# Performance work log

Hardware: AMD Instinct MI355X
Metric: run time of the kernel (lower is better)

The kernel has to match this reference:

```python
import jax, jax.numpy as jnp
import numpy as np

FP8_E4M3_MAX = 448.0  # torch.float8_e4m3fn max


def _fp8_quant(x, scale):
    # per-tensor static-scale fp8 quantization: clamp(x/scale) -> e4m3 -> back to f32
    q = jnp.clip(x / scale, -FP8_E4M3_MAX, FP8_E4M3_MAX)
    return q.astype(jnp.float8_e4m3fn).astype(jnp.float32)


def setup_inputs() -> dict:
    key = jax.random.key(0)
    k1, k2, k3 = jax.random.split(key, 3)
    M, K, N = 8192, 4096, 11008
    inp = jax.random.normal(k1, (M, K), dtype=jnp.float32)
    # weight is stored pre-quantized (fp8 values held as fp32), already transposed to [K, N]
    w = jax.random.normal(k2, (K, N), dtype=jnp.float32) * 0.02
    weight_scale = jnp.float32(0.01)
    qweight = _fp8_quant(w, weight_scale)
    qbias = jax.random.normal(k3, (N,), dtype=jnp.float32) * 0.01
    input_scale = jnp.float32(0.05)
    return {
        "input": inp,
        "qweight": qweight,
        "qbias": qbias,
        "weight_scale": weight_scale,
        "input_scale": input_scale,
    }


def reference(input, qweight, qbias, weight_scale, input_scale) -> jnp.ndarray:
    # scaled_fp8_quant with a provided static scale: x_scale == input_scale
    qinput = _fp8_quant(input, input_scale)  # [M, K], fp8 values in f32
    # cutlass_scaled_mm / _scaled_mm: (qinput * x_scale) @ (qweight * weight_scale) + bias
    out = jnp.einsum("mk,kn->mn", qinput, qweight) * (input_scale * weight_scale)
    out = out + qbias[None, :]
    return out.astype(input.dtype)
```

## Files before the change

kernel.cpp:

```cpp
#include <hip/hip_runtime.h>

typedef float v4f __attribute__((ext_vector_type(4)));
typedef unsigned long long u64x2 __attribute__((ext_vector_type(2)));

#define BM 128
#define BN 128
#define BK 64

__device__ __forceinline__ unsigned int pack4_fp8(float a, float b, float c, float d) {
    unsigned int v = __builtin_amdgcn_cvt_pk_fp8_f32(a, b, 0, false);
    v = __builtin_amdgcn_cvt_pk_fp8_f32(c, d, v, true);
    return v;
}

__global__ __launch_bounds__(256) void quant_x_kernel(
    const float* __restrict__ X, const float* __restrict__ sp,
    unsigned int* __restrict__ Q)
{
    const long i = (long)blockIdx.x * 256 + threadIdx.x;
    const float s = sp[0];
    const float4 v = ((const float4*)X)[i];
    const float a = fminf(fmaxf(v.x / s, -448.f), 448.f);
    const float b = fminf(fmaxf(v.y / s, -448.f), 448.f);
    const float c = fminf(fmaxf(v.z / s, -448.f), 448.f);
    const float d = fminf(fmaxf(v.w / s, -448.f), 448.f);
    Q[i] = pack4_fp8(a, b, c, d);
}

__global__ __launch_bounds__(256) void quant_wT_kernel(
    const float* __restrict__ Wf, unsigned char* __restrict__ Wq, int K, int N)
{
    const int k0 = blockIdx.x * 64;
    const int n0 = blockIdx.y * 64;
    const int t  = threadIdx.x;
    const int n  = t >> 2;
    const int kc = (t & 3) * 16;
    const float* src = Wf + (long)(k0 + kc) * N + n0 + n;
    unsigned int o[4];
#pragma unroll
    for (int j = 0; j < 4; ++j) {
        const float x0 = src[(long)(4 * j + 0) * N];
        const float x1 = src[(long)(4 * j + 1) * N];
        const float x2 = src[(long)(4 * j + 2) * N];
        const float x3 = src[(long)(4 * j + 3) * N];
        o[j] = pack4_fp8(x0, x1, x2, x3);
    }
    uint4 q; q.x = o[0]; q.y = o[1]; q.z = o[2]; q.w = o[3];
    *(uint4*)(Wq + (long)(n0 + n) * K + k0 + kc) = q;
}

__device__ __forceinline__ void async_copy16(const void* g, void* l) {
    __builtin_amdgcn_global_load_lds(
        (const __attribute__((address_space(1))) unsigned int*)g,
        (__attribute__((address_space(3))) unsigned int*)l,
        16, 0, 0);
}

__global__ __launch_bounds__(256) void fp8_gemm_kernel(
    const unsigned char* __restrict__ A8,
    const unsigned char* __restrict__ B8,
    const float* __restrict__ bias,
    const float* __restrict__ ws_p, const float* __restrict__ is_p,
    float* __restrict__ C, int M, int N, int K)
{
    __shared__ unsigned long long As[BM * BK / 8];
    __shared__ unsigned long long Bs[BN * BK / 8];

    const int tid = threadIdx.x;
    const int l   = tid & 63;
    const int w   = tid >> 6;
    const int wr  = w >> 1, wc = w & 1;
    const int lm  = l & 15, lg = l >> 4;

    const long m0 = (long)blockIdx.y * BM;
    const long n0 = (long)blockIdx.x * BN;

    const unsigned char* aG = A8 + (m0 + (tid >> 2)) * (long)K + (tid & 3) * 16;
    const unsigned char* bG = B8 + (n0 + (tid >> 2)) * (long)K + (tid & 3) * 16;
    const long rowStep = (long)64 * K;

    unsigned char* AsB = (unsigned char*)As;
    unsigned char* BsB = (unsigned char*)Bs;
    const u64x2* As2 = (const u64x2*)As;
    const u64x2* Bs2 = (const u64x2*)Bs;

    v4f acc[4][4];
#pragma unroll
    for (int i = 0; i < 4; ++i)
#pragma unroll
        for (int j = 0; j < 4; ++j)
            acc[i][j] = (v4f){0.f, 0.f, 0.f, 0.f};

    for (int kt = 0; kt < K; kt += BK) {
        async_copy16(aG + kt,           AsB + tid * 16);
        async_copy16(aG + kt + rowStep, AsB + 4096 + tid * 16);
        async_copy16(bG + kt,           BsB + tid * 16);
        async_copy16(bG + kt + rowStep, BsB + 4096 + tid * 16);
        __syncthreads();

        u64x2 a[4], b[4];
#pragma unroll
        for (int mt = 0; mt < 4; ++mt)
            a[mt] = As2[(wr * 64 + mt * 16 + lm) * 4 + lg];
#pragma unroll
        for (int nt = 0; nt < 4; ++nt)
            b[nt] = Bs2[(wc * 64 + nt * 16 + lm) * 4 + lg];

#pragma unroll
        for (int mt = 0; mt < 4; ++mt)
#pragma unroll
            for (int nt = 0; nt < 4; ++nt) {
                acc[mt][nt] = __builtin_amdgcn_mfma_f32_16x16x32_fp8_fp8(
                    (long)a[mt][0], (long)b[nt][0], acc[mt][nt], 0, 0, 0);
                acc[mt][nt] = __builtin_amdgcn_mfma_f32_16x16x32_fp8_fp8(
                    (long)a[mt][1], (long)b[nt][1], acc[mt][nt], 0, 0, 0);
            }
        __syncthreads();
    }

    const float s = is_p[0] * ws_p[0];
#pragma unroll
    for (int nt = 0; nt < 4; ++nt) {
        const long c = n0 + wc * 64 + nt * 16 + lm;
        const float bv = bias[c];
#pragma unroll
        for (int mt = 0; mt < 4; ++mt) {
            const long r = m0 + wr * 64 + mt * 16 + lg * 4;
            float* dst = C + r * (long)N + c;
#pragma unroll
            for (int i = 0; i < 4; ++i)
                dst[(long)i * N] = acc[mt][nt][i] * s + bv;
        }
    }
}

extern "C" void kernel_launch(void* const* d_in, const int* in_sizes, int n_in,
                              void* d_out, int out_size, void* d_ws, size_t ws_size,
                              hipStream_t stream)
{
    const float* X    = (const float*)d_in[0];
    const float* Wf   = (const float*)d_in[1];
    const float* bias = (const float*)d_in[2];
    const float* wsc  = (const float*)d_in[3];
    const float* isc  = (const float*)d_in[4];
    float* out = (float*)d_out;

    const int N = in_sizes[2];
    const int K = in_sizes[1] / N;
    const int M = in_sizes[0] / K;

    unsigned char* A8 = (unsigned char*)d_ws;
    unsigned char* B8 = A8 + (size_t)M * K;

    quant_x_kernel<<<dim3((unsigned)((long)M * K / 4 / 256)), 256, 0, stream>>>(
        X, isc, (unsigned int*)A8);

    quant_wT_kernel<<<dim3(K / 64, N / 64), 256, 0, stream>>>(Wf, B8, K, N);

    fp8_gemm_kernel<<<dim3(N / BN, M / BM), 256, 0, stream>>>(
        A8, B8, bias, wsc, isc, out, M, N, K);
}
```

Measured before the change: 1.241 ms.

## Switch GEMM to 32x32x64 scaled FP8 MFMA with XOR-swizzled LDS layout

Replaces the 16x16x32 fp8 MFMA tiles with the gfx950 32x32x64 f8f6f4 scaled MFMA, using unit scales, so each wave issues 4 larger MFMAs per K-tile instead of 32 small ones. The LDS tile is stored with an XOR swizzle on 16-byte chunks, matched on the global-to-LDS copy side, so the 32-byte-per-lane fragment reads avoid bank conflicts. The output write pattern is remapped to the 32x32 accumulator layout. It relies on the correct fragment and accumulator layout for the new instruction.

```diff
diff --git a/kernel.cpp b/kernel.cpp
--- a/kernel.cpp
+++ b/kernel.cpp
@@ -1,7 +1,8 @@
 #include <hip/hip_runtime.h>
 
-typedef float v4f __attribute__((ext_vector_type(4)));
-typedef unsigned long long u64x2 __attribute__((ext_vector_type(2)));
+typedef float v16f __attribute__((ext_vector_type(16)));
+typedef int   v8i  __attribute__((ext_vector_type(8)));
+typedef int   v4i  __attribute__((ext_vector_type(4)));
 
 #define BM 128
 #define BN 128
@@ -56,6 +57,16 @@
         16, 0, 0);
 }
 
+__device__ __forceinline__ v8i ld_frag(const unsigned char* base, int row, int c0) {
+    const int sw = (row >> 1) & 3;
+    const v4i lo = *(const v4i*)(base + row * 64 + (((c0    ) ^ sw) << 4));
+    const v4i hi = *(const v4i*)(base + row * 64 + (((c0 + 1) ^ sw) << 4));
+    v8i f;
+    f[0] = lo[0]; f[1] = lo[1]; f[2] = lo[2]; f[3] = lo[3];
+    f[4] = hi[0]; f[5] = hi[1]; f[6] = hi[2]; f[7] = hi[3];
+    return f;
+}
+
 __global__ __launch_bounds__(256) void fp8_gemm_kernel(
     const unsigned char* __restrict__ A8,
     const unsigned char* __restrict__ B8,
@@ -63,33 +74,33 @@
     const float* __restrict__ ws_p, const float* __restrict__ is_p,
     float* __restrict__ C, int M, int N, int K)
 {
-    __shared__ unsigned long long As[BM * BK / 8];
-    __shared__ unsigned long long Bs[BN * BK / 8];
+    __shared__ unsigned char AsB[BM * BK];
+    __shared__ unsigned char BsB[BN * BK];
 
     const int tid = threadIdx.x;
     const int l   = tid & 63;
     const int w   = tid >> 6;
     const int wr  = w >> 1, wc = w & 1;
-    const int lm  = l & 15, lg = l >> 4;
+    const int lrow = l & 31;
+    const int c0   = (l >> 5) * 2;
 
     const long m0 = (long)blockIdx.y * BM;
     const long n0 = (long)blockIdx.x * BN;
 
-    const unsigned char* aG = A8 + (m0 + (tid >> 2)) * (long)K + (tid & 3) * 16;
-    const unsigned char* bG = B8 + (n0 + (tid >> 2)) * (long)K + (tid & 3) * 16;
+    const int srow = tid >> 2;
+    const int sch  = (tid & 3) ^ ((tid >> 3) & 3);
+    const unsigned char* aG = A8 + (m0 + srow) * (long)K + sch * 16;
+    const unsigned char* bG = B8 + (n0 + srow) * (long)K + sch * 16;
     const long rowStep = (long)64 * K;
 
-    unsigned char* AsB = (unsigned char*)As;
-    unsigned char* BsB = (unsigned char*)Bs;
-    const u64x2* As2 = (const u64x2*)As;
-    const u64x2* Bs2 = (const u64x2*)Bs;
-
-    v4f acc[4][4];
+    v16f acc[2][2];
 #pragma unroll
-    for (int i = 0; i < 4; ++i)
+    for (int i = 0; i < 2; ++i)
 #pragma unroll
-        for (int j = 0; j < 4; ++j)
-            acc[i][j] = (v4f){0.f, 0.f, 0.f, 0.f};
+        for (int j = 0; j < 2; ++j)
+#pragma unroll
+            for (int e = 0; e < 16; ++e)
+                acc[i][j][e] = 0.f;
 
     for (int kt = 0; kt < K; kt += BK) {
         async_copy16(aG + kt,           AsB + tid * 16);
@@ -98,40 +109,40 @@
         async_copy16(bG + kt + rowStep, BsB + 4096 + tid * 16);
         __syncthreads();
 
-        u64x2 a[4], b[4];
+        v8i a[2], b[2];
 #pragma unroll
-        for (int mt = 0; mt < 4; ++mt)
-            a[mt] = As2[(wr * 64 + mt * 16 + lm) * 4 + lg];
+        for (int mt = 0; mt < 2; ++mt)
+            a[mt] = ld_frag(AsB, wr * 64 + mt * 32 + lrow, c0);
 #pragma unroll
-        for (int nt = 0; nt < 4; ++nt)
-            b[nt] = Bs2[(wc * 64 + nt * 16 + lm) * 4 + lg];
+        for (int nt = 0; nt < 2; ++nt)
+            b[nt] = ld_frag(BsB, wc * 64 + nt * 32 + lrow, c0);
 
 #pragma unroll
-        for (int mt = 0; mt < 4; ++mt)
+        for (int mt = 0; mt < 2; ++mt)
 #pragma unroll
-            for (int nt = 0; nt < 4; ++nt) {
-                acc[mt][nt] = __builtin_amdgcn_mfma_f32_16x16x32_fp8_fp8(
-                    (long)a[mt][0], (long)b[nt][0], acc[mt][nt], 0, 0, 0);
-                acc[mt][nt] = __builtin_amdgcn_mfma_f32_16x16x32_fp8_fp8(
-                    (long)a[mt][1], (long)b[nt][1], acc[mt][nt], 0, 0, 0);
-            }
+            for (int nt = 0; nt < 2; ++nt)
+                acc[mt][nt] = __builtin_amdgcn_mfma_scale_f32_32x32x64_f8f6f4(
+                    a[mt], b[nt], acc[mt][nt],
+                    0 , 0 ,
+                    0, 0x7F7F7F7Fu ,
+                    0, 0x7F7F7F7Fu );
         __syncthreads();
     }
 
     const float s = is_p[0] * ws_p[0];
 #pragma unroll
-    for (int nt = 0; nt < 4; ++nt) {
-        const long c = n0 + wc * 64 + nt * 16 + lm;
-        const float bv = bias[c];
+    for (int mt = 0; mt < 2; ++mt)
 #pragma unroll
-        for (int mt = 0; mt < 4; ++mt) {
-            const long r = m0 + wr * 64 + mt * 16 + lg * 4;
-            float* dst = C + r * (long)N + c;
+        for (int nt = 0; nt < 2; ++nt) {
+            const long cc = n0 + wc * 64 + nt * 32 + lrow;
+            const float bv = bias[cc];
+            float* dst = C + (m0 + wr * 64 + mt * 32 + (l >> 5) * 4) * (long)N + cc;
 #pragma unroll
-            for (int i = 0; i < 4; ++i)
-                dst[(long)i * N] = acc[mt][nt][i] * s + bv;
+            for (int g = 0; g < 4; ++g)
+#pragma unroll
+                for (int r = 0; r < 4; ++r)
+                    dst[(long)(g * 8 + r) * N] = acc[mt][nt][g * 4 + r] * s + bv;
         }
-    }
 }
 
 extern "C" void kernel_launch(void* const* d_in, const int* in_sizes, int n_in,
```

After: 1.109 ms. 10.7% less time.
